# Kernel tuning notes

Hardware: AMD Instinct MI355X
Metric: run time of the kernel (lower is better)

## Reference

```python
import jax, jax.numpy as jnp
import numpy as np

MUL = 32            # multiplicity of each irrep (0e and 1o)
N_NODES = 50000
N_EDGES = 800000
NUM_NEIGHBORS = 16.0
SQRT3 = 3.0 ** 0.5
SILU_NORM = 1.6790  # e3nn normalize2mom constant for silu: 1/sqrt(E[silu(z)^2]), z~N(0,1)


def split_irreps(x):
    # x: [..., 128] laid out as 32x0e (32) ++ 32x1o (32*3)
    x0 = x[..., :MUL]
    x1 = x[..., MUL:].reshape(x.shape[:-1] + (MUL, 3))
    return x0, x1


def merge_irreps(x0, x1):
    return jnp.concatenate([x0, x1.reshape(x1.shape[:-2] + (MUL * 3,))], axis=-1)


def fctp_scalar(x0, x1, a, W0, W1, fan_in):
    # FullyConnectedTensorProduct(in_irreps, '1x0e', out_irreps): per-irrep linear
    # mixing scaled by scalar attr; e3nn path weight sqrt(dim_out/fan_in) times the
    # orthonormal CG (1/sqrt(dim)) folds to 1/sqrt(fan_in) for every irrep.
    s = a / jnp.sqrt(jnp.asarray(fan_in, x0.dtype))
    o0 = (x0 @ W0) * s
    o1 = jnp.einsum('nud,uw->nwd', x1, W1) * s[..., None]
    return o0, o1


def setup_inputs() -> dict:
    key = jax.random.key(0)
    ks = jax.random.split(key, 17)
    inp = dict(
        node_input=jax.random.normal(ks[0], (N_NODES, 4 * MUL), jnp.float32),
        node_attr=jnp.ones((N_NODES, 1), jnp.float32),
        edge_src=jax.random.randint(ks[1], (N_EDGES,), 0, N_NODES),
        edge_dst=jax.random.randint(ks[2], (N_EDGES,), 0, N_NODES),
        edge_attr=jax.random.normal(ks[3], (N_EDGES, 4), jnp.float32),
        edge_scalars=jax.random.normal(ks[4], (N_EDGES, 64), jnp.float32),
    )
    p = lambda k, sh: jax.random.normal(k, sh, jnp.float32)  # e3nn init: N(0,1)
    inp.update(
        W_sc0=p(ks[5], (MUL, MUL)), W_sc1=p(ks[6], (MUL, MUL)),
        W_l1_0=p(ks[7], (MUL, MUL)), W_l1_1=p(ks[8], (MUL, MUL)),
        W_fc1=p(ks[9], (64, 64)), W_fc2=p(ks[10], (64, 4 * MUL)),
        W_l2_A0=p(ks[11], (MUL, MUL)), W_l2_B0=p(ks[12], (MUL, MUL)),
        W_l2_C1=p(ks[13], (MUL, MUL)), W_l2_D1=p(ks[14], (MUL, MUL)),
        W_l3_A=p(ks[15], (MUL, 1)), W_l3_B=p(ks[16], (MUL, 1)),
    )
    return inp


def reference(node_input, node_attr, edge_src, edge_dst, edge_attr, edge_scalars,
              W_sc0, W_sc1, W_l1_0, W_l1_1, W_fc1, W_fc2,
              W_l2_A0, W_l2_B0, W_l2_C1, W_l2_D1, W_l3_A, W_l3_B):
    n = node_input.shape[0]
    x0, x1 = split_irreps(node_input)

    # per-edge TP weights from MLP on edge scalars (e3nn FullyConnectedNet)
    h = SILU_NORM * jax.nn.silu(edge_scalars @ (W_fc1 / 8.0))  # /sqrt(64)
    weight = h @ (W_fc2 / 8.0)                                  # [E, 128]

    # self connection (sc) and lin1 (FCTP with scalar node attr, fan_in = 32)
    sc0, sc1 = fctp_scalar(x0, x1, node_attr, W_sc0, W_sc1, MUL)
    f0, f1 = fctp_scalar(x0, x1, node_attr, W_l1_0, W_l1_1, MUL)

    # gather source-node features per edge
    g0 = f0[edge_src]          # [E, 32]
    g1 = f1[edge_src]          # [E, 32, 3]
    e0 = edge_attr[:, :1]      # [E, 1]  0e
    e1 = edge_attr[:, 1:]      # [E, 3]  1o

    # weight layout follows instruction order: (0e*0e->0e), (0e*1o->1o), (1o*0e->1o), (1o*1o->0e)
    wA, wC, wD, wB = (weight[:, :MUL], weight[:, MUL:2 * MUL],
                      weight[:, 2 * MUL:3 * MUL], weight[:, 3 * MUL:])
    # weighted CG tensor product ('uvu'); e3nn path weights sqrt(dim_out) folded with
    # orthonormal wigner-3j entries (1/sqrt(3) for l=1 couplings)
    outA = wA * g0 * e0                                    # [E,32]   0e x 0e -> 0e
    outB = wB * jnp.einsum('euk,ek->eu', g1, e1) / SQRT3   # [E,32]   1o x 1o -> 0e
    outC = (wC * g0)[..., None] * e1[:, None, :]           # [E,32,3] 0e x 1o -> 1o
    outD = wD[..., None] * g1 * e0[..., None]              # [E,32,3] 1o x 0e -> 1o

    # scatter-add aggregation to destination nodes
    seg = lambda v: jax.ops.segment_sum(v, edge_dst, num_segments=n)
    inv = 1.0 / jnp.sqrt(jnp.asarray(NUM_NEIGHBORS, node_input.dtype))
    mA, mB, mC, mD = seg(outA) * inv, seg(outB) * inv, seg(outC) * inv, seg(outD) * inv

    # lin2: irreps_mid (32x0e+32x0e+32x1o+32x1o) -> output, fan_in = 64 per output irrep
    s = node_attr / 8.0  # attr / sqrt(64)
    c0 = (mA @ W_l2_A0 + mB @ W_l2_B0) * s
    c1 = (jnp.einsum('nud,uw->nwd', mC, W_l2_C1)
          + jnp.einsum('nud,uw->nwd', mD, W_l2_D1)) * s[..., None]

    # lin3: irreps_mid -> 0e gate angle (only 0e chunks contribute)
    angle = 0.1 * (mA @ W_l3_A + mB @ W_l3_B) * s          # [N, 1]
    cos, sin = jnp.cos(angle), jnp.sin(angle)              # sc.output_mask is all ones

    return cos * merge_irreps(sc0, sc1) + sin * merge_irreps(c0, c1)
```

## Files before the change

kernel.cpp:

```cpp
#include <hip/hip_runtime.h>
#include <stdint.h>

#define N_NODES 50000
#define N_EDGES 800000
#define CAP 64
#define NTILES 50000
#define NSB 49

typedef _Float16 f16x8 __attribute__((ext_vector_type(8)));
typedef _Float16 f16x2 __attribute__((ext_vector_type(2)));
typedef float    f32x4 __attribute__((ext_vector_type(4)));

static __device__ __forceinline__ uint32_t pk16(float a, float b) {
    return __builtin_bit_cast(uint32_t, __builtin_amdgcn_cvt_pkrtz(a, b));
}
static __device__ __forceinline__ float lo16(uint32_t v) {
    f16x2 h = __builtin_bit_cast(f16x2, v); return (float)h[0];
}
static __device__ __forceinline__ float hi16(uint32_t v) {
    f16x2 h = __builtin_bit_cast(f16x2, v); return (float)h[1];
}

__global__ __launch_bounds__(256) void k_node_f(
        const float* __restrict__ x, const float* __restrict__ attr,
        const float* __restrict__ W0, const float* __restrict__ W1,
        uint32_t* __restrict__ fh)
{
    const int wv = threadIdx.x >> 6;
    const int t  = threadIdx.x & 63;
    const int node = blockIdx.x*4 + wv;
    if (node >= N_NODES) return;
    __shared__ float xs[4][128];
    xs[wv][t]      = x[(size_t)node*128 + t];
    xs[wv][64 + t] = x[(size_t)node*128 + 64 + t];
    float a = attr[node] * 0.17677669529663689f;
    float s0 = 0.f, s1 = 0.f;
    if (t < 32) {
        #pragma unroll
        for (int v = 0; v < 32; ++v) {
            s0 += xs[wv][v] * W0[v*32 + t];
            s1 += xs[wv][32 + v*3 + 0] * W1[v*32 + t];
        }
    } else {
        int u = t - 32;
        #pragma unroll
        for (int v = 0; v < 32; ++v) {
            s0 += xs[wv][32 + v*3 + 1] * W1[v*32 + u];
            s1 += xs[wv][32 + v*3 + 2] * W1[v*32 + u];
        }
    }
    fh[(size_t)node*64 + t] = pk16(s0*a, s1*a);
}

__global__ void k_ticket(const int* __restrict__ dst, int* __restrict__ cnt,
                         uint8_t* __restrict__ slot8) {
    int e = blockIdx.x*256 + threadIdx.x;
    if (e >= N_EDGES) return;
    int d = dst[e];
    int slot = atomicAdd(&cnt[d], 1);
    slot8[e] = (uint8_t)min(slot, 255);
}

__global__ __launch_bounds__(1024) void k_scan1(const int* __restrict__ cnt,
                                                int* __restrict__ offs,
                                                int* __restrict__ bsum) {
    __shared__ int sh[1024];
    int t = threadIdx.x, i = blockIdx.x*1024 + t;
    int v = (i < N_NODES) ? min(cnt[i], CAP) : 0;
    sh[t] = v; __syncthreads();
    #pragma unroll
    for (int off = 1; off < 1024; off <<= 1) {
        int u = (t >= off) ? sh[t - off] : 0;
        __syncthreads();
        sh[t] += u;
        __syncthreads();
    }
    if (i < N_NODES) offs[i] = sh[t] - v;
    if (t == 1023) bsum[blockIdx.x] = sh[t];
}

__global__ void k_scan2(const int* __restrict__ bsum, int* __restrict__ bbase,
                        int* __restrict__ offs) {
    int t = threadIdx.x;
    int v = (t < NSB) ? bsum[t] : 0;
    int inc = v;
    #pragma unroll
    for (int off = 1; off < 64; off <<= 1) {
        int u = __shfl_up(inc, off);
        if (t >= off) inc += u;
    }
    if (t < NSB) bbase[t] = inc - v;
    if (t == NSB - 1) offs[N_NODES] = inc;
}

__global__ __launch_bounds__(1024) void k_scan3(int* __restrict__ offs,
                                                const int* __restrict__ bbase) {
    int i = blockIdx.x*1024 + threadIdx.x;
    if (i < N_NODES) offs[i] += bbase[blockIdx.x];
}

__global__ void k_scatter(const int* __restrict__ dst, const int* __restrict__ esrc,
                          const float* __restrict__ eattr,
                          const uint8_t* __restrict__ slot8,
                          const int* __restrict__ offs,
                          int2* __restrict__ csr_se, float4* __restrict__ csr_e1) {
    int e = blockIdx.x*256 + threadIdx.x;
    if (e >= N_EDGES) return;
    int slot = slot8[e];
    if (slot >= CAP) return;
    int pos = offs[dst[e]] + slot;
    csr_se[pos] = make_int2(e, esrc[e]);
    float4 ea = *(const float4*)(eattr + (size_t)e*4);
    csr_e1[pos] = make_float4(ea.y, ea.z, ea.w, ea.x);
}

__global__ __launch_bounds__(256) void k_edge_w(
    const float* __restrict__ escal,
    const float* __restrict__ Wfc1, const float* __restrict__ Wfc2,
    const int2* __restrict__ csr_se, const float4* __restrict__ csr_e1,
    const int* __restrict__ offs, uint32_t* __restrict__ weight)
{
    __shared__ __align__(16) _Float16 lds_h[4][16][72];
    __shared__ __align__(16) uint32_t lds_o[4][16][64];

    const int wv   = threadIdx.x >> 6;
    const int lane = threadIdx.x & 63;
    const int rl   = lane & 15;
    const int g4   = lane >> 4;

    f16x8 w1f[2][4];
    #pragma unroll
    for (int ks = 0; ks < 2; ++ks)
      #pragma unroll
      for (int jt = 0; jt < 4; ++jt)
        #pragma unroll
        for (int i = 0; i < 8; ++i)
          w1f[ks][jt][i] = (_Float16)(Wfc1[(ks*32 + g4*8 + i)*64 + jt*16 + rl] * 0.125f);
    f16x8 w2f[2][8];
    #pragma unroll
    for (int ks = 0; ks < 2; ++ks)
      #pragma unroll
      for (int jt = 0; jt < 8; ++jt)
        #pragma unroll
        for (int i = 0; i < 8; ++i)
          w2f[ks][jt][i] = (_Float16)(Wfc2[(ks*32 + g4*8 + i)*128 + jt*16 + rl] * 0.125f);

    const int Ptot = offs[N_NODES];
    const int w  = blockIdx.x*4 + wv;
    const int t0 = w*8;
    const int t1 = (t0 + 8 < NTILES) ? t0 + 8 : NTILES;

    for (int tt = t0; tt < t1; ++tt) {
        const int p0 = tt*16;
        if (p0 >= Ptot) break;
        const int rows = min(16, Ptot - p0);
        const int pr = p0 + min(rl, rows - 1);
        const int eL = csr_se[pr].x;
        const float e0L = csr_e1[pr].w;

        f16x8 af[2];
        #pragma unroll
        for (int ks = 0; ks < 2; ++ks) {
            const float* p = escal + (size_t)eL*64 + ks*32 + g4*8;
            float4 lo = *(const float4*)(p);
            float4 hi = *(const float4*)(p + 4);
            af[ks][0]=(_Float16)lo.x; af[ks][1]=(_Float16)lo.y;
            af[ks][2]=(_Float16)lo.z; af[ks][3]=(_Float16)lo.w;
            af[ks][4]=(_Float16)hi.x; af[ks][5]=(_Float16)hi.y;
            af[ks][6]=(_Float16)hi.z; af[ks][7]=(_Float16)hi.w;
        }

        f32x4 hacc[4];
        #pragma unroll
        for (int jt = 0; jt < 4; ++jt) {
            f32x4 z = {0.f,0.f,0.f,0.f};
            z = __builtin_amdgcn_mfma_f32_16x16x32_f16(af[0], w1f[0][jt], z, 0,0,0);
            z = __builtin_amdgcn_mfma_f32_16x16x32_f16(af[1], w1f[1][jt], z, 0,0,0);
            hacc[jt] = z;
        }
        #pragma unroll
        for (int jt = 0; jt < 4; ++jt)
          #pragma unroll
          for (int r = 0; r < 4; ++r) {
            float v = hacc[jt][r];
            float s = 1.679f * v / (1.f + __expf(-v));
            lds_h[wv][g4*4 + r][jt*16 + rl] = (_Float16)s;
          }
        f16x8 a2[2];
        #pragma unroll
        for (int ks = 0; ks < 2; ++ks)
            a2[ks] = *reinterpret_cast<const f16x8*>(&lds_h[wv][rl][ks*32 + g4*8]);

        f32x4 z[8];
        #pragma unroll
        for (int jt = 0; jt < 8; ++jt) {
            f32x4 zz = {0.f,0.f,0.f,0.f};
            zz = __builtin_amdgcn_mfma_f32_16x16x32_f16(a2[0], w2f[0][jt], zz, 0,0,0);
            zz = __builtin_amdgcn_mfma_f32_16x16x32_f16(a2[1], w2f[1][jt], zz, 0,0,0);
            z[jt] = zz;
        }

        #pragma unroll
        for (int pg = 0; pg < 2; ++pg)
          #pragma unroll
          for (int r = 0; r < 4; ++r) {
            float e0r = __shfl(e0L, g4*4 + r);
            float loA = z[pg][r]     * (0.25f * e0r);
            float hiC = z[2 + pg][r] * 0.25f;
            float loD = z[4 + pg][r] * (0.25f * e0r);
            float hiB = z[6 + pg][r] * 0.14433756729740643f;
            lds_o[wv][g4*4 + r][pg*16 + rl]      = pk16(loA, hiC);
            lds_o[wv][g4*4 + r][32 + pg*16 + rl] = pk16(loD, hiB);
          }

        const int qr = lane >> 4;
        const int ql = lane & 15;
        #pragma unroll
        for (int it = 0; it < 4; ++it) {
            int r = it*4 + qr;
            if (r < rows) {
                *(uint4*)(weight + (size_t)(p0 + r)*64 + ql*4) =
                    *(const uint4*)(&lds_o[wv][r][ql*4]);
            }
        }
    }
}

__global__ __launch_bounds__(256, 6) void k_main(
    const float* __restrict__ x, const float* __restrict__ attr,
    const uint32_t* __restrict__ weight, const int2* __restrict__ csr_se,
    const float4* __restrict__ csr_e1,
    const float* __restrict__ Wsc0, const float* __restrict__ Wsc1,
    const float* __restrict__ WA0,  const float* __restrict__ WB0,
    const float* __restrict__ WC1,  const float* __restrict__ WD1,
    const float* __restrict__ W3A,  const float* __restrict__ W3B,
    const uint32_t* __restrict__ fh, const int* __restrict__ offs,
    float* __restrict__ out)
{
    __shared__ float lds_m[4][256];

    const int wv   = threadIdx.x >> 6;
    const int lane = threadIdx.x & 63;
    const int u    = lane & 31;
    const int half = lane >> 5;
    const int node = blockIdx.x*4 + wv;
    if (node >= N_NODES) return;

    const int o0  = __builtin_amdgcn_readfirstlane(offs[node]);
    const int deg = __builtin_amdgcn_readfirstlane(offs[node + 1]) - o0;

    float mAB = 0.f, mCD0 = 0.f, mCD1 = 0.f, mCD2 = 0.f;

    for (int b = 0; b < deg; b += 16) {
        int nb = min(16, deg - b);
        uint32_t wp[16], ga[16], gbv[16];
        #pragma unroll
        for (int j = 0; j < 16; ++j) if (j < nb) {
            int pos = o0 + b + j;
            int sm = csr_se[pos].y;
            wp[j] = weight[(size_t)pos*64 + lane];
            const uint32_t* fr = fh + (size_t)sm*64;
            ga[j] = fr[u];
            if (half) gbv[j] = fr[32 + u];
        }
        #pragma unroll
        for (int j = 0; j < 16; ++j) if (j < nb) {
            int pos = o0 + b + j;
            float4 v = csr_e1[pos];
            float e1x = v.x, e1y = v.y, e1z = v.z;
            float lo = lo16(wp[j]), hi = hi16(wp[j]);
            if (half == 0) {
                float g0 = lo16(ga[j]);
                mAB += lo * g0;
                float tc = hi * g0;
                mCD0 += tc*e1x; mCD1 += tc*e1y; mCD2 += tc*e1z;
            } else {
                float gx = hi16(ga[j]);
                float gy = lo16(gbv[j]), gz = hi16(gbv[j]);
                mAB += hi * (gx*e1x + gy*e1y + gz*e1z);
                mCD0 += lo*gx; mCD1 += lo*gy; mCD2 += lo*gz;
            }
        }
    }

    float* M = lds_m[wv];
    if (half == 0) {
        M[u] = mAB;
        M[64  + u*3 + 0] = mCD0; M[64  + u*3 + 1] = mCD1; M[64  + u*3 + 2] = mCD2;
    } else {
        M[32 + u] = mAB;
        M[160 + u*3 + 0] = mCD0; M[160 + u*3 + 1] = mCD1; M[160 + u*3 + 2] = mCD2;
    }

    float a    = attr[node];
    float a8   = a * 0.125f;
    float as32 = a * 0.17677669529663689f;

    const float w3 = (half == 0) ? W3A[u] : W3B[u];
    float tpart = (half == 0) ? M[u] * w3 : M[32 + u] * w3;
    #pragma unroll
    for (int off = 32; off > 0; off >>= 1) tpart += __shfl_xor(tpart, off);
    float angle = 0.1f * tpart * a8;
    float sn, cs; __sincosf(angle, &sn, &cs);

    const float* xr = x + (size_t)node*128;
    #pragma unroll
    for (int pass = 0; pass < 2; ++pass) {
        int c = lane + pass*64;
        bool A = (c < 32);
        int cc = c - 32;
        int wq = cc / 3, d = cc - 3*wq;
        int sT = A ? 1 : 3;
        const float* pT1 = A ? &M[0]        : &M[64 + d];
        const float* pT2 = A ? &M[32]       : &M[160 + d];
        const float* pX  = A ? xr           : xr + 32 + d;
        int k = A ? c : wq;
        const float* pWa = (A ? WA0  : WC1)  + k;
        const float* pWb = (A ? WB0  : WD1)  + k;
        const float* pWx = (A ? Wsc0 : Wsc1) + k;
        float s1 = 0.f, s2 = 0.f;
        #pragma unroll
        for (int uu = 0; uu < 32; ++uu) {
            s1 += pT1[uu*sT] * pWa[uu*32] + pT2[uu*sT] * pWb[uu*32];
            s2 += pX[uu*sT]  * pWx[uu*32];
        }
        out[(size_t)node*128 + c] = cs*(s2*as32) + sn*(s1*a8);
    }
}

extern "C" void kernel_launch(void* const* d_in, const int* in_sizes, int n_in,
                              void* d_out, int out_size, void* d_ws, size_t ws_size,
                              hipStream_t stream) {
    const float* node_input = (const float*)d_in[0];
    const float* node_attr  = (const float*)d_in[1];
    const int*   edge_src   = (const int*)  d_in[2];
    const int*   edge_dst   = (const int*)  d_in[3];
    const float* edge_attr  = (const float*)d_in[4];
    const float* edge_scal  = (const float*)d_in[5];
    const float* W_sc0 = (const float*)d_in[6];
    const float* W_sc1 = (const float*)d_in[7];
    const float* W_l10 = (const float*)d_in[8];
    const float* W_l11 = (const float*)d_in[9];
    const float* W_fc1 = (const float*)d_in[10];
    const float* W_fc2 = (const float*)d_in[11];
    const float* W_A0  = (const float*)d_in[12];
    const float* W_B0  = (const float*)d_in[13];
    const float* W_C1  = (const float*)d_in[14];
    const float* W_D1  = (const float*)d_in[15];
    const float* W_3A  = (const float*)d_in[16];
    const float* W_3B  = (const float*)d_in[17];
    float* out = (float*)d_out;

    char* p = (char*)d_ws;
    auto alloc = [&](size_t bytes) { char* r = p; p += (bytes + 15) & ~(size_t)15; return r; };
    uint32_t* fh      = (uint32_t*)alloc((size_t)N_NODES*64*4);
    int*      cnt     = (int*)     alloc((size_t)N_NODES*4);
    int*      offs    = (int*)     alloc((size_t)(N_NODES+1)*4);
    uint8_t*  slot8   = (uint8_t*) alloc((size_t)N_EDGES);
    int*      bsum    = (int*)     alloc((size_t)NSB*4);
    int*      bbase   = (int*)     alloc((size_t)NSB*4);
    int2*     csr_se  = (int2*)    alloc((size_t)N_EDGES*8);
    float4*   csr_e1  = (float4*)  alloc((size_t)N_EDGES*16);
    uint32_t* weight  = (uint32_t*)alloc((size_t)N_EDGES*64*4);

    hipMemsetAsync(cnt, 0, (size_t)N_NODES*4, stream);
    k_node_f <<<(N_NODES+3)/4, 256, 0, stream>>>(node_input, node_attr, W_l10, W_l11, fh);
    k_ticket <<<(N_EDGES+255)/256, 256, 0, stream>>>(edge_dst, cnt, slot8);
    k_scan1  <<<NSB, 1024, 0, stream>>>(cnt, offs, bsum);
    k_scan2  <<<1, 64, 0, stream>>>(bsum, bbase, offs);
    k_scan3  <<<NSB, 1024, 0, stream>>>(offs, bbase);
    k_scatter<<<(N_EDGES+255)/256, 256, 0, stream>>>(edge_dst, edge_src, edge_attr,
               slot8, offs, csr_se, csr_e1);
    k_edge_w <<<1563, 256, 0, stream>>>(edge_scal, W_fc1, W_fc2, csr_se, csr_e1, offs, weight);
    k_main   <<<(N_NODES+3)/4, 256, 0, stream>>>(node_input, node_attr, weight, csr_se, csr_e1,
               W_sc0, W_sc1, W_A0, W_B0, W_C1, W_D1, W_3A, W_3B, fh, offs, out);
}
```

Measured before the change: 401.1 us.

## Move source-feature gather and per-edge products into edge-weight kernel

The edge kernel now gathers the source node features and forms the per-edge tensor-product contributions itself, writing a 96-word fp16 contribution per edge instead of the 64-word weight. The main kernel then only streams these contributions and sums them, no longer doing random gathers from the node-feature table. This moves the irregular gather into the edge stage, where it sits next to the MFMA work. The cost is a larger intermediate buffer (more bytes written and read per edge) and an extra fp16 rounding of the products.

```diff
diff --git a/kernel.cpp b/kernel.cpp
--- a/kernel.cpp
+++ b/kernel.cpp
@@ -114,11 +114,12 @@
     csr_e1[pos] = make_float4(ea.y, ea.z, ea.w, ea.x);
 }
 
-__global__ __launch_bounds__(256) void k_edge_w(
+__global__ __launch_bounds__(256) void k_edge_c(
     const float* __restrict__ escal,
     const float* __restrict__ Wfc1, const float* __restrict__ Wfc2,
     const int2* __restrict__ csr_se, const float4* __restrict__ csr_e1,
-    const int* __restrict__ offs, uint32_t* __restrict__ weight)
+    const int* __restrict__ offs, const uint32_t* __restrict__ fh,
+    uint32_t* __restrict__ contrib)
 {
     __shared__ __align__(16) _Float16 lds_h[4][16][72];
     __shared__ __align__(16) uint32_t lds_o[4][16][64];
@@ -127,6 +128,8 @@
     const int lane = threadIdx.x & 63;
     const int rl   = lane & 15;
     const int g4   = lane >> 4;
+    const int u    = lane & 31;
+    const int half = lane >> 5;
 
     f16x8 w1f[2][4];
     #pragma unroll
@@ -213,14 +216,36 @@
             lds_o[wv][g4*4 + r][32 + pg*16 + rl] = pk16(loD, hiB);
           }
 
-        const int qr = lane >> 4;
-        const int ql = lane & 15;
-        #pragma unroll
-        for (int it = 0; it < 4; ++it) {
-            int r = it*4 + qr;
-            if (r < rows) {
-                *(uint4*)(weight + (size_t)(p0 + r)*64 + ql*4) =
-                    *(const uint4*)(&lds_o[wv][r][ql*4]);
+        for (int bb = 0; bb < rows; bb += 8) {
+            int nb = min(8, rows - bb);
+            uint32_t ga[8], gb2[8];
+            #pragma unroll
+            for (int j = 0; j < 8; ++j) if (j < nb) {
+                int pos = p0 + bb + j;
+                int sm = csr_se[pos].y;
+                const uint32_t* fr = fh + (size_t)sm*64;
+                ga[j] = fr[u];
+                if (half) gb2[j] = fr[32 + u];
+            }
+            #pragma unroll
+            for (int j = 0; j < 8; ++j) if (j < nb) {
+                int mm = bb + j;
+                int pos = p0 + mm;
+                size_t base = (size_t)pos * 96;
+                if (half == 0) {
+                    uint32_t wAC = lds_o[wv][mm][u];
+                    float g0 = lo16(ga[j]);
+                    contrib[base + u] = pk16(lo16(wAC)*g0, hi16(wAC)*g0);
+                } else {
+                    uint32_t wDB = lds_o[wv][mm][32 + u];
+                    float4 ev = csr_e1[pos];
+                    float g1x = hi16(ga[j]);
+                    float g1y = lo16(gb2[j]), g1z = hi16(gb2[j]);
+                    float wD_ = lo16(wDB), wB_ = hi16(wDB);
+                    float cB = wB_ * (g1x*ev.x + g1y*ev.y + g1z*ev.z);
+                    *(uint2*)(contrib + base + 32 + 2*u) =
+                        make_uint2(pk16(cB, wD_*g1x), pk16(wD_*g1y, wD_*g1z));
+                }
             }
         }
     }
@@ -228,14 +253,12 @@
 
 __global__ __launch_bounds__(256, 6) void k_main(
     const float* __restrict__ x, const float* __restrict__ attr,
-    const uint32_t* __restrict__ weight, const int2* __restrict__ csr_se,
-    const float4* __restrict__ csr_e1,
+    const uint32_t* __restrict__ contrib, const float4* __restrict__ csr_e1,
     const float* __restrict__ Wsc0, const float* __restrict__ Wsc1,
     const float* __restrict__ WA0,  const float* __restrict__ WB0,
     const float* __restrict__ WC1,  const float* __restrict__ WD1,
     const float* __restrict__ W3A,  const float* __restrict__ W3B,
-    const uint32_t* __restrict__ fh, const int* __restrict__ offs,
-    float* __restrict__ out)
+    const int* __restrict__ offs,   float* __restrict__ out)
 {
     __shared__ float lds_m[4][256];
 
@@ -253,32 +276,25 @@
 
     for (int b = 0; b < deg; b += 16) {
         int nb = min(16, deg - b);
-        uint32_t wp[16], ga[16], gbv[16];
+        uint2 cv[16];
         #pragma unroll
         for (int j = 0; j < 16; ++j) if (j < nb) {
-            int pos = o0 + b + j;
-            int sm = csr_se[pos].y;
-            wp[j] = weight[(size_t)pos*64 + lane];
-            const uint32_t* fr = fh + (size_t)sm*64;
-            ga[j] = fr[u];
-            if (half) gbv[j] = fr[32 + u];
+            size_t base = (size_t)(o0 + b + j) * 96;
+            if (half == 0) cv[j].x = contrib[base + u];
+            else           cv[j]   = *(const uint2*)(contrib + base + 32 + 2*u);
         }
         #pragma unroll
         for (int j = 0; j < 16; ++j) if (j < nb) {
-            int pos = o0 + b + j;
-            float4 v = csr_e1[pos];
-            float e1x = v.x, e1y = v.y, e1z = v.z;
-            float lo = lo16(wp[j]), hi = hi16(wp[j]);
             if (half == 0) {
-                float g0 = lo16(ga[j]);
-                mAB += lo * g0;
-                float tc = hi * g0;
-                mCD0 += tc*e1x; mCD1 += tc*e1y; mCD2 += tc*e1z;
+                float4 ev = csr_e1[o0 + b + j];
+                mAB += lo16(cv[j].x);
+                float tC = hi16(cv[j].x);
+                mCD0 += tC*ev.x; mCD1 += tC*ev.y; mCD2 += tC*ev.z;
             } else {
-                float gx = hi16(ga[j]);
-                float gy = lo16(gbv[j]), gz = hi16(gbv[j]);
-                mAB += hi * (gx*e1x + gy*e1y + gz*e1z);
-                mCD0 += lo*gx; mCD1 += lo*gy; mCD2 += lo*gz;
+                mAB  += lo16(cv[j].x);
+                mCD0 += hi16(cv[j].x);
+                mCD1 += lo16(cv[j].y);
+                mCD2 += hi16(cv[j].y);
             }
         }
     }
@@ -361,7 +377,7 @@
     int*      bbase   = (int*)     alloc((size_t)NSB*4);
     int2*     csr_se  = (int2*)    alloc((size_t)N_EDGES*8);
     float4*   csr_e1  = (float4*)  alloc((size_t)N_EDGES*16);
-    uint32_t* weight  = (uint32_t*)alloc((size_t)N_EDGES*64*4);
+    uint32_t* contrib = (uint32_t*)alloc((size_t)N_EDGES*96*4);
 
     hipMemsetAsync(cnt, 0, (size_t)N_NODES*4, stream);
     k_node_f <<<(N_NODES+3)/4, 256, 0, stream>>>(node_input, node_attr, W_l10, W_l11, fh);
@@ -371,7 +387,8 @@
     k_scan3  <<<NSB, 1024, 0, stream>>>(offs, bbase);
     k_scatter<<<(N_EDGES+255)/256, 256, 0, stream>>>(edge_dst, edge_src, edge_attr,
                slot8, offs, csr_se, csr_e1);
-    k_edge_w <<<1563, 256, 0, stream>>>(edge_scal, W_fc1, W_fc2, csr_se, csr_e1, offs, weight);
-    k_main   <<<(N_NODES+3)/4, 256, 0, stream>>>(node_input, node_attr, weight, csr_se, csr_e1,
-               W_sc0, W_sc1, W_A0, W_B0, W_C1, W_D1, W_3A, W_3B, fh, offs, out);
-}
+    k_edge_c <<<1563, 256, 0, stream>>>(edge_scal, W_fc1, W_fc2, csr_se, csr_e1,
+               offs, fh, contrib);
+    k_main   <<<(N_NODES+3)/4, 256, 0, stream>>>(node_input, node_attr, contrib, csr_e1,
+               W_sc0, W_sc1, W_A0, W_B0, W_C1, W_D1, W_3A, W_3B, offs, out);
+}
```

Result: slower. 867.4 us (+116.3%).

## Compute edge MLP weights in original edge order and gather them in main kernel

Applied to the files above, without the earlier changes.

The edge MLP kernel now processes edges in their original order, reading edge scalars and attributes contiguously and writing weight tiles with fully coalesced stores, with no dependency on CSR arrays. The main aggregation kernel instead indexes weights by original edge id taken from csr_se. This trades the gather of edge scalars in the MLP kernel for a random 256-byte-row gather of weights in the main kernel, and it also computes weights for edges dropped by the per-node cap.

```diff
diff --git a/kernel.cpp b/kernel.cpp
--- a/kernel.cpp
+++ b/kernel.cpp
@@ -115,10 +115,9 @@
 }
 
 __global__ __launch_bounds__(256) void k_edge_w(
-    const float* __restrict__ escal,
+    const float* __restrict__ escal, const float* __restrict__ eattr,
     const float* __restrict__ Wfc1, const float* __restrict__ Wfc2,
-    const int2* __restrict__ csr_se, const float4* __restrict__ csr_e1,
-    const int* __restrict__ offs, uint32_t* __restrict__ weight)
+    uint32_t* __restrict__ weight)
 {
     __shared__ __align__(16) _Float16 lds_h[4][16][72];
     __shared__ __align__(16) uint32_t lds_o[4][16][64];
@@ -145,23 +144,16 @@
         for (int i = 0; i < 8; ++i)
           w2f[ks][jt][i] = (_Float16)(Wfc2[(ks*32 + g4*8 + i)*128 + jt*16 + rl] * 0.125f);
 
-    const int Ptot = offs[N_NODES];
     const int w  = blockIdx.x*4 + wv;
     const int t0 = w*8;
     const int t1 = (t0 + 8 < NTILES) ? t0 + 8 : NTILES;
 
     for (int tt = t0; tt < t1; ++tt) {
-        const int p0 = tt*16;
-        if (p0 >= Ptot) break;
-        const int rows = min(16, Ptot - p0);
-        const int pr = p0 + min(rl, rows - 1);
-        const int eL = csr_se[pr].x;
-        const float e0L = csr_e1[pr].w;
-
+        const int eb = tt*16;
         f16x8 af[2];
         #pragma unroll
         for (int ks = 0; ks < 2; ++ks) {
-            const float* p = escal + (size_t)eL*64 + ks*32 + g4*8;
+            const float* p = escal + (size_t)(eb + rl)*64 + ks*32 + g4*8;
             float4 lo = *(const float4*)(p);
             float4 hi = *(const float4*)(p + 4);
             af[ks][0]=(_Float16)lo.x; af[ks][1]=(_Float16)lo.y;
@@ -169,6 +161,7 @@
             af[ks][4]=(_Float16)hi.x; af[ks][5]=(_Float16)hi.y;
             af[ks][6]=(_Float16)hi.z; af[ks][7]=(_Float16)hi.w;
         }
+        float e0L = eattr[(size_t)(eb + rl)*4];
 
         f32x4 hacc[4];
         #pragma unroll
@@ -213,15 +206,11 @@
             lds_o[wv][g4*4 + r][32 + pg*16 + rl] = pk16(loD, hiB);
           }
 
-        const int qr = lane >> 4;
-        const int ql = lane & 15;
-        #pragma unroll
-        for (int it = 0; it < 4; ++it) {
-            int r = it*4 + qr;
-            if (r < rows) {
-                *(uint4*)(weight + (size_t)(p0 + r)*64 + ql*4) =
-                    *(const uint4*)(&lds_o[wv][r][ql*4]);
-            }
+        uint32_t* wg = weight + (size_t)eb*64;
+        const uint32_t* lo32 = &lds_o[wv][0][0];
+        #pragma unroll
+        for (int pq = 0; pq < 4; ++pq) {
+            *(uint4*)(wg + pq*256 + lane*4) = *(const uint4*)(lo32 + pq*256 + lane*4);
         }
     }
 }
@@ -257,9 +246,9 @@
         #pragma unroll
         for (int j = 0; j < 16; ++j) if (j < nb) {
             int pos = o0 + b + j;
-            int sm = csr_se[pos].y;
-            wp[j] = weight[(size_t)pos*64 + lane];
-            const uint32_t* fr = fh + (size_t)sm*64;
+            int2 se = csr_se[pos];
+            wp[j] = weight[(size_t)se.x*64 + lane];
+            const uint32_t* fr = fh + (size_t)se.y*64;
             ga[j] = fr[u];
             if (half) gbv[j] = fr[32 + u];
         }
@@ -371,7 +360,7 @@
     k_scan3  <<<NSB, 1024, 0, stream>>>(offs, bbase);
     k_scatter<<<(N_EDGES+255)/256, 256, 0, stream>>>(edge_dst, edge_src, edge_attr,
                slot8, offs, csr_se, csr_e1);
-    k_edge_w <<<1563, 256, 0, stream>>>(edge_scal, W_fc1, W_fc2, csr_se, csr_e1, offs, weight);
+    k_edge_w <<<1563, 256, 0, stream>>>(edge_scal, edge_attr, W_fc1, W_fc2, weight);
     k_main   <<<(N_NODES+3)/4, 256, 0, stream>>>(node_input, node_attr, weight, csr_se, csr_e1,
                W_sc0, W_sc1, W_A0, W_B0, W_C1, W_D1, W_3A, W_3B, fh, offs, out);
 }
```

Result: faster. 389.2 us (-3.0%).
